# Kernel tuning notes

Measured on AMD Instinct MI355X. Metric: run time of the kernel, lower is better.

The kernel has to match this reference:

```python
import jax, jax.numpy as jnp
import numpy as np

B, N, DIM, H, DH = 2, 1024, 1024, 8, 64
DI = H * DH  # 512
K = 4        # depthwise conv kernel
EPS = 1.1920929e-07  # float32 eps (torch RMSNorm default)


def setup_inputs() -> dict:
    key = jax.random.key(0)
    ks = jax.random.split(key, 12)
    s = lambda k, shape, sc=0.02: jax.random.normal(k, shape, jnp.float32) * sc
    return dict(
        x=jax.random.normal(ks[0], (B, N, DIM), jnp.float32),
        w_rms=jnp.ones((DIM,), jnp.float32),
        wq=s(ks[1], (DIM, DI)), wk=s(ks[2], (DIM, DI)), wv=s(ks[3], (DIM, DI)),
        wo=s(ks[4], (DI, DIM)),
        conv_q=s(ks[5], (DIM, K), 0.3), conv_k=s(ks[6], (DIM, K), 0.3), conv_v=s(ks[7], (DIM, K), 0.3),
        gamma_q=jnp.ones((H, 1, DH), jnp.float32), gamma_k=jnp.ones((H, 1, DH), jnp.float32),
        lr_w=s(ks[8], (DIM, H)), lr_b=jnp.full((H,), -4.0, jnp.float32),
        decay_w=s(ks[9], (DIM, H)), decay_b=jnp.full((H,), 4.0, jnp.float32),
        mom_w=s(ks[10], (DIM, H)), mom_b=jnp.full((H,), 2.0, jnp.float32),
    )


def rmsnorm(x, w):
    return x * jax.lax.rsqrt(jnp.mean(x * x, -1, keepdims=True) + EPS) * w


def mh_rmsnorm(x, gamma):  # x: (b, h, n, d)
    rms = jnp.sqrt(jnp.sum(x * x, -1, keepdims=True)) * (DH ** -0.5)
    return x / jnp.maximum(rms, 1e-8) * gamma


def dwconv(x, w):  # x: (b, n, dim), w: (dim, K) depthwise, padding K//2 -> length n+1
    y = jax.lax.conv_general_dilated(
        x.transpose(0, 2, 1), w[:, None, :], (1,), [(K // 2, K // 2)],
        feature_group_count=DIM, dimension_numbers=('NCW', 'OIW', 'NCW'))
    return y.transpose(0, 2, 1)


def gated_scan(a, x):  # h_t = a_t h_{t-1} + x_t, h_{-1}=0; a:(bh,t), x:(bh,t,d,d)
    def combine(c1, c2):
        a1, x1 = c1
        a2, x2 = c2
        return a1 * a2, a2 * x1 + x2
    _, h = jax.lax.associative_scan(combine, (a[..., None, None], x), axis=1)
    return h


def reference(x, w_rms, wq, wk, wv, wo, conv_q, conv_k, conv_v,
              gamma_q, gamma_k, lr_w, lr_b, decay_w, decay_b, mom_w, mom_b):
    b, n, _ = x.shape
    xa = rmsnorm(x, w_rms)
    qi, ki, vi = dwconv(xa, conv_q), dwconv(xa, conv_k), dwconv(xa, conv_v)
    split = lambda t: t.reshape(b, -1, H, DH).transpose(0, 2, 1, 3)[:, :, :n]  # (b,h,n,d)
    q = mh_rmsnorm(split(qi @ wq), gamma_q)
    k = mh_rmsnorm(split(ki @ wk), gamma_k)
    v = split(vi @ wv)
    fq = q.reshape(b * H, n, DH)
    fk = k.reshape(b * H, n, DH)
    fv = v.reshape(b * H, n, DH)
    sig = jax.nn.sigmoid
    lr = sig(xa @ lr_w + lr_b).transpose(0, 2, 1).reshape(b * H, n)
    decay = sig(xa @ decay_w + decay_b).transpose(0, 2, 1).reshape(b * H, n)
    mom = sig(xa @ mom_w + mom_b).transpose(0, 2, 1).reshape(b * H, n)
    # S_ref = S0 = 0 (fresh state) => pred = 0, delta_vec = -v
    g = jnp.einsum('bti,btj->btij', -fv, fk)          # (bh, n, d, d)
    Z = gated_scan(mom, g)                             # momentum scan
    S = gated_scan(decay, -lr[..., None, None] * Z)    # memory scan
    S_prev = jnp.concatenate([jnp.zeros_like(S[:, :1]), S[:, :-1]], axis=1)
    y = jnp.einsum('btdp,btp->btd', S_prev, fq)        # retrieval y_t = S_{t-1} psi_t
    y = y.reshape(b, H, n, DH).transpose(0, 2, 1, 3).reshape(b, n, DI)
    return y @ wo
```

## Files before the change

kernel.cpp:

```cpp
#include <hip/hip_runtime.h>
#include <math.h>

#define DEV __device__ __forceinline__

constexpr int Bb   = 2;
constexpr int Seq  = 1024;
constexpr int Dim  = 1024;
constexpr int Hh   = 8;
constexpr int Dh   = 64;
constexpr int Di   = 512;
constexpr int BN   = Bb * Seq;
constexpr int NSEQ = Bb * Hh;
constexpr int CHUNK = 32;
constexpr int CLEN  = Seq / CHUNK;
constexpr float EPSV = 1.1920929e-07f;
constexpr int NT2  = 8;
constexpr int KSPL = 8;

typedef _Float16 half8 __attribute__((ext_vector_type(8)));
typedef float    f32x4 __attribute__((ext_vector_type(4)));

DEV float bf2f(unsigned short u) {
  union { unsigned int i; float f; } x; x.i = ((unsigned int)u) << 16; return x.f;
}
DEV unsigned short f2bf(float f) {
  union { float f; unsigned int i; } x; x.f = f;
  unsigned int r = x.i + 0x7fffu + ((x.i >> 16) & 1u);
  return (unsigned short)(r >> 16);
}
DEV float ldin(const void* p, int f32, size_t i) {
  if (f32) return ((const float*)p)[i];
  return bf2f(((const unsigned short*)p)[i]);
}
DEV void ld4(const void* p, int f32, size_t i, float* dst) {
  if (f32) {
    float4 u = *(const float4*)((const float*)p + i);
    dst[0] = u.x; dst[1] = u.y; dst[2] = u.z; dst[3] = u.w;
  } else {
    ushort4 u = *(const ushort4*)((const unsigned short*)p + i);
    dst[0] = bf2f(u.x); dst[1] = bf2f(u.y); dst[2] = bf2f(u.z); dst[3] = bf2f(u.w);
  }
}
DEV int sniff_vote(const void* p, int n, int tid) {
  int j = 2 * tid, valid = 0, bad = 0;
  if (j < n) {
    valid = 1;
    float v = bf2f(((const unsigned short*)p)[j]);
    float a = fabsf(v);
    if (!(a >= 1e-12f && a <= 1e4f)) bad = 1;
  }
#pragma unroll
  for (int m = 1; m < 64; m <<= 1) { valid += __shfl_xor(valid, m); bad += __shfl_xor(bad, m); }
  return (2 * bad > valid) ? 1 : 0;
}

DEV void gld16(const _Float16* g, _Float16* l) {
  __builtin_amdgcn_global_load_lds(
      (const __attribute__((address_space(1))) void*)g,
      (__attribute__((address_space(3))) void*)l, 16, 0, 0);
}

struct InPtrs { const void* p[17]; int n[17]; };

__global__ __launch_bounds__(256) void k_front(
    InPtrs ip,
    int* __restrict__ flags,
    _Float16* __restrict__ wqT, _Float16* __restrict__ wkT,
    _Float16* __restrict__ wvT, _Float16* __restrict__ woT,
    _Float16* __restrict__ WgT,
    float* __restrict__ gqf, float* __restrict__ gkf, float* __restrict__ gbf,
    _Float16* __restrict__ xaf,
    _Float16* __restrict__ qc, _Float16* __restrict__ kc,
    _Float16* __restrict__ vc)
{
  int blk = blockIdx.x;
  int tid = threadIdx.x;
  __shared__ int sfl[8];
  __shared__ __align__(16) char smem_u[11 * Dim * 2];

  if (blk < 1024) {
    int z = blk >> 8, bx = blk & 15, by = (blk >> 4) & 15;
    int idx = (z == 0) ? 2 : ((z == 1) ? 3 : ((z == 2) ? 4 : 5));
    const void* src = ip.p[idx];
    _Float16* dst   = (z == 0) ? wqT : ((z == 1) ? wkT : ((z == 2) ? wvT : woT));
    int Kd = (z < 3) ? Dim : Di;
    int Nn = (z < 3) ? Di : Dim;
    int n0 = bx * 64, k0 = by * 64;
    if (n0 >= Nn || k0 >= Kd) return;

    if (tid < 64) { int f = sniff_vote(src, ip.n[idx], tid); if (tid == 0) sfl[0] = f; }
    __syncthreads();
    int f = sfl[0];

    float (*tile)[65] = (float(*)[65])smem_u;
    int r = tid >> 4, c4 = (tid & 15) * 4;
#pragma unroll
    for (int rr = 0; rr < 4; ++rr) {
      int k = rr * 16 + r;
      ld4(src, f, (size_t)(k0 + k) * Nn + n0 + c4, &tile[k][c4]);
    }
    __syncthreads();
#pragma unroll
    for (int rr = 0; rr < 4; ++rr) {
      int n = rr * 16 + r;
      _Float16 o4[4];
#pragma unroll
      for (int j = 0; j < 4; ++j) o4[j] = (_Float16)tile[c4 + j][n];
      *(ushort4*)&dst[(size_t)(n0 + n) * Kd + k0 + c4] = *(ushort4*)o4;
    }
  } else if (blk < 1088) {
    int row = blk - 1024;
    if (row < 24) {
      int g = row >> 3, h = row & 7;
      int idx = (g == 0) ? 11 : ((g == 1) ? 13 : 15);
      const void* W = ip.p[idx];
      if (tid < 64) { int f = sniff_vote(W, ip.n[idx], tid); if (tid == 0) sfl[0] = f; }
      __syncthreads();
      int f = sfl[0];
#pragma unroll
      for (int it = 0; it < 4; ++it) {
        int d = it * 256 + tid;
        WgT[(size_t)row * Dim + d] = (_Float16)ldin(W, f, (size_t)d * Hh + h);
      }
    } else {
#pragma unroll
      for (int it = 0; it < 4; ++it)
        WgT[(size_t)row * Dim + it * 256 + tid] = (_Float16)0.f;
    }
  } else if (blk == 1088) {
    __shared__ int allf[17];
    for (int ii = 0; ii < 17; ++ii) {
      if (tid < 64) {
        int f = sniff_vote(ip.p[ii], ip.n[ii], tid);
        if (tid == 0) { flags[ii] = f; allf[ii] = f; }
      }
    }
    __syncthreads();
    int f9 = allf[9], f10 = allf[10];
    for (int i = tid; i < Di; i += 256) {
      gqf[i] = ldin(ip.p[9], f9, i);
      gkf[i] = ldin(ip.p[10], f10, i);
    }
    if (tid < 24) {
      int g = tid >> 3, h = tid & 7;
      int idx = (g == 0) ? 12 : ((g == 1) ? 14 : 16);
      gbf[tid] = ldin(ip.p[idx], allf[idx], h);
    }
  } else {
    constexpr int NR = NT2 + 3;
    _Float16 (*xas)[Dim] = (_Float16(*)[Dim])smem_u;

    int rb = blk - 1089;
    int tb = rb & 127, b = rb >> 7;
    int t0 = tb * NT2;
    int lane = tid & 63, wv = tid >> 6;

    if (tid < 64) {
      int f0 = sniff_vote(ip.p[0], ip.n[0], tid);
      int f1 = sniff_vote(ip.p[1], ip.n[1], tid);
      int f6 = sniff_vote(ip.p[6], ip.n[6], tid);
      int f7 = sniff_vote(ip.p[7], ip.n[7], tid);
      int f8 = sniff_vote(ip.p[8], ip.n[8], tid);
      if (tid == 0) { sfl[0] = f0; sfl[1] = f1; sfl[2] = f6; sfl[3] = f7; sfl[4] = f8; }
    }
    __syncthreads();
    int fx = sfl[0], fw = sfl[1], f6 = sfl[2], f7 = sfl[3], f8 = sfl[4];
    int e0 = lane * 16;

    float wr[16];
#pragma unroll
    for (int q = 0; q < 4; ++q) ld4(ip.p[1], fw, e0 + q * 4, &wr[q * 4]);

    for (int rr = wv; rr < NR; rr += 4) {
      int r = t0 - 2 + rr;
      float xv[16];
      bool inr = (r >= 0 && r < Seq);
      if (inr) {
        size_t rbx = (size_t)(b * Seq + r) * Dim + e0;
#pragma unroll
        for (int q = 0; q < 4; ++q) ld4(ip.p[0], fx, rbx + q * 4, &xv[q * 4]);
      } else {
#pragma unroll
        for (int j = 0; j < 16; ++j) xv[j] = 0.f;
      }
      float ss = 0.f;
#pragma unroll
      for (int j = 0; j < 16; ++j) ss = fmaf(xv[j], xv[j], ss);
#pragma unroll
      for (int m = 1; m < 64; m <<= 1) ss += __shfl_xor(ss, m);
      float scale = rsqrtf(ss * (1.0f / Dim) + EPSV);

      _Float16 o[16];
#pragma unroll
      for (int j = 0; j < 16; ++j) o[j] = (_Float16)(xv[j] * scale * wr[j]);
      *(uint4*)&xas[rr][e0]     = *(uint4*)&o[0];
      *(uint4*)&xas[rr][e0 + 8] = *(uint4*)&o[8];
      if (inr && r >= t0 && r < t0 + NT2) {
        size_t ob = (size_t)(b * Seq + r) * Dim + e0;
        *(uint4*)&xaf[ob]     = *(uint4*)&o[0];
        *(uint4*)&xaf[ob + 8] = *(uint4*)&o[8];
      }
    }
    __syncthreads();

    int c0 = tid * 4;
    float lwq[16], lwk[16], lwv[16];
#pragma unroll
    for (int q = 0; q < 4; ++q) {
      ld4(ip.p[6], f6, (size_t)c0 * 4 + q * 4, &lwq[q * 4]);
      ld4(ip.p[7], f7, (size_t)c0 * 4 + q * 4, &lwk[q * 4]);
      ld4(ip.p[8], f8, (size_t)c0 * 4 + q * 4, &lwv[q * 4]);
    }

#pragma unroll
    for (int tt = 0; tt < NT2; ++tt) {
      float rv[4][4];
#pragma unroll
      for (int k = 0; k < 4; ++k) {
        _Float16 hx[4];
        *(ushort4*)hx = *(const ushort4*)&xas[tt + k][c0];
#pragma unroll
        for (int j = 0; j < 4; ++j) rv[k][j] = (float)hx[j];
      }
      _Float16 tq[4], tk[4], tv[4];
#pragma unroll
      for (int j = 0; j < 4; ++j) {
        float aq = rv[0][j] * lwq[j * 4 + 0] + rv[1][j] * lwq[j * 4 + 1]
                 + rv[2][j] * lwq[j * 4 + 2] + rv[3][j] * lwq[j * 4 + 3];
        float ak = rv[0][j] * lwk[j * 4 + 0] + rv[1][j] * lwk[j * 4 + 1]
                 + rv[2][j] * lwk[j * 4 + 2] + rv[3][j] * lwk[j * 4 + 3];
        float av = rv[0][j] * lwv[j * 4 + 0] + rv[1][j] * lwv[j * 4 + 1]
                 + rv[2][j] * lwv[j * 4 + 2] + rv[3][j] * lwv[j * 4 + 3];
        tq[j] = (_Float16)aq; tk[j] = (_Float16)ak; tv[j] = (_Float16)av;
      }
      size_t o = ((size_t)(b * Seq + t0 + tt)) * Dim + c0;
      *(ushort4*)&qc[o] = *(ushort4*)tq;
      *(ushort4*)&kc[o] = *(ushort4*)tk;
      *(ushort4*)&vc[o] = *(ushort4*)tv;
    }
  }
}

__global__ __launch_bounds__(256) void k_mid(
    const _Float16* __restrict__ qc, const _Float16* __restrict__ kc,
    const _Float16* __restrict__ vc,
    const _Float16* __restrict__ wqT, const _Float16* __restrict__ wkT,
    const _Float16* __restrict__ wvT,
    const _Float16* __restrict__ xaf, const _Float16* __restrict__ WgT,
    _Float16* __restrict__ qpre, _Float16* __restrict__ kpre,
    _Float16* __restrict__ vpre,
    float* __restrict__ gpart)
{
  __shared__ __align__(16) _Float16 ldsbuf[256 * 64];

  int blk = blockIdx.x;
  int tid = threadIdx.x, lane = tid & 63, wv = tid >> 6;
  int mrow = lane & 15, quad = lane >> 4;

  if (blk < 192) {
    int z = blk >> 6, rem = blk & 63;
    int by = rem >> 2, bx = rem & 3;
    const _Float16* A  = (z == 0) ? qc : ((z == 1) ? kc : vc);
    const _Float16* Bt = (z == 0) ? wqT : ((z == 1) ? wkT : wvT);
    _Float16* C        = (z == 0) ? qpre : ((z == 1) ? kpre : vpre);
    int m0 = by * 128, n0 = bx * 128;
    int wr = wv >> 1, wc = wv & 1;

    _Float16* Asl = ldsbuf;
    _Float16* Bsl = ldsbuf + 128 * 64;

    int sr8 = lane >> 3;
    int sc8 = (lane & 7) * 8;

    f32x4 acc[4][4];
#pragma unroll
    for (int mi = 0; mi < 4; ++mi)
#pragma unroll
      for (int ni = 0; ni < 4; ++ni) acc[mi][ni] = (f32x4){0.f, 0.f, 0.f, 0.f};

    for (int kt = 0; kt < Dim; kt += 64) {
      __syncthreads();
#pragma unroll
      for (int u = 0; u < 4; ++u) {
        int r0 = wv * 32 + u * 8;
        gld16(&A [(size_t)(m0 + r0 + sr8) * Dim + kt + sc8], &Asl[r0 * 64]);
        gld16(&Bt[(size_t)(n0 + r0 + sr8) * Dim + kt + sc8], &Bsl[r0 * 64]);
      }
      __syncthreads();

#pragma unroll
      for (int kh = 0; kh < 2; ++kh) {
        half8 afr[4], bfr[4];
#pragma unroll
        for (int i = 0; i < 4; ++i)
          afr[i] = *(const half8*)&Asl[(wr * 64 + i * 16 + mrow) * 64 + kh * 32 + quad * 8];
#pragma unroll
        for (int i = 0; i < 4; ++i)
          bfr[i] = *(const half8*)&Bsl[(wc * 64 + i * 16 + mrow) * 64 + kh * 32 + quad * 8];
#pragma unroll
        for (int mi = 0; mi < 4; ++mi)
#pragma unroll
          for (int ni = 0; ni < 4; ++ni)
            acc[mi][ni] = __builtin_amdgcn_mfma_f32_16x16x32_f16(afr[mi], bfr[ni], acc[mi][ni], 0, 0, 0);
      }
    }

#pragma unroll
    for (int mi = 0; mi < 4; ++mi) {
#pragma unroll
      for (int ni = 0; ni < 4; ++ni) {
        int col = n0 + wc * 64 + ni * 16 + mrow;
#pragma unroll
        for (int r2 = 0; r2 < 4; ++r2) {
          int row = m0 + wr * 64 + mi * 16 + quad * 4 + r2;
          C[(size_t)row * Di + col] = (_Float16)acc[mi][ni][r2];
        }
      }
    }
  } else {
    _Float16 (*As)[40] = (_Float16(*)[40])ldsbuf;
    _Float16 (*Bs)[40] = (_Float16(*)[40])(ldsbuf + 128 * 40);

    int g = blk - 192;
    int m0 = (g & 31) * 64, ks = g >> 5;
    int srow = tid >> 2, scol = (tid & 3) * 8;
    int kbase = ks * (Dim / KSPL);

    f32x4 acc[4];
#pragma unroll
    for (int mi = 0; mi < 4; ++mi) acc[mi] = (f32x4){0.f, 0.f, 0.f, 0.f};

    for (int kt = kbase; kt < kbase + Dim / KSPL; kt += 32) {
      __syncthreads();
      *(uint4*)&As[srow][scol] = *(const uint4*)&xaf[(size_t)(m0 + srow) * Dim + kt + scol];
      *(uint4*)&Bs[srow][scol] = *(const uint4*)&WgT[(size_t)srow * Dim + kt + scol];
      __syncthreads();
      half8 bfr = *(const half8*)&Bs[wv * 16 + mrow][quad * 8];
#pragma unroll
      for (int mi = 0; mi < 4; ++mi) {
        half8 afr = *(const half8*)&As[mi * 16 + mrow][quad * 8];
        acc[mi] = __builtin_amdgcn_mfma_f32_16x16x32_f16(afr, bfr, acc[mi], 0, 0, 0);
      }
    }

    int col = wv * 16 + mrow;
    if (col < 24) {
#pragma unroll
      for (int mi = 0; mi < 4; ++mi) {
#pragma unroll
        for (int r2 = 0; r2 < 4; ++r2) {
          int row = m0 + mi * 16 + quad * 4 + r2;
          gpart[((size_t)ks * BN + row) * 32 + col] = acc[mi][r2];
        }
      }
    }
  }
}

__global__ __launch_bounds__(256) void k_gemm_fin(
    const _Float16* __restrict__ A, const _Float16* __restrict__ Bt,
    void* __restrict__ C, const int* __restrict__ flags, int Nn, int Kd)
{
  __shared__ __align__(16) _Float16 lds[(64 + 64) * 32];
  _Float16* Asl = lds;
  _Float16* Bsl = lds + 64 * 32;

  int tid = threadIdx.x, lane = tid & 63, wv = tid >> 6;
  int n0 = blockIdx.x * 64, m0 = blockIdx.y * 64;
  int mrow = lane & 15, quad = lane >> 4;
  int wr = wv >> 1, wc = wv & 1;
  int sr = lane >> 2, sc = (lane & 3) * 8;

  f32x4 acc[2][2];
#pragma unroll
  for (int mi = 0; mi < 2; ++mi)
#pragma unroll
    for (int ni = 0; ni < 2; ++ni) acc[mi][ni] = (f32x4){0.f, 0.f, 0.f, 0.f};

  for (int kt = 0; kt < Kd; kt += 32) {
    __syncthreads();
    gld16(&A [(size_t)(m0 + wv * 16 + sr) * Kd + kt + sc], &Asl[(wv * 16) * 32]);
    gld16(&Bt[(size_t)(n0 + wv * 16 + sr) * Kd + kt + sc], &Bsl[(wv * 16) * 32]);
    __syncthreads();

    half8 afr[2], bfr[2];
#pragma unroll
    for (int i2 = 0; i2 < 2; ++i2) {
      afr[i2] = *(const half8*)&Asl[(wr * 32 + i2 * 16 + mrow) * 32 + quad * 8];
      bfr[i2] = *(const half8*)&Bsl[(wc * 32 + i2 * 16 + mrow) * 32 + quad * 8];
    }
#pragma unroll
    for (int mi = 0; mi < 2; ++mi)
#pragma unroll
      for (int ni = 0; ni < 2; ++ni)
        acc[mi][ni] = __builtin_amdgcn_mfma_f32_16x16x32_f16(afr[mi], bfr[ni], acc[mi][ni], 0, 0, 0);
  }

  int any_bf16 = 0;
#pragma unroll
  for (int i2 = 0; i2 < 17; ++i2) any_bf16 |= (flags[i2] == 0);

#pragma unroll
  for (int mi = 0; mi < 2; ++mi) {
#pragma unroll
    for (int ni = 0; ni < 2; ++ni) {
      int col = n0 + wc * 32 + ni * 16 + mrow;
#pragma unroll
      for (int r2 = 0; r2 < 4; ++r2) {
        int row = m0 + wr * 32 + mi * 16 + quad * 4 + r2;
        float v = acc[mi][ni][r2];
        size_t idx = (size_t)row * Nn + col;
        if (any_bf16) ((unsigned short*)C)[idx] = f2bf(v);
        else          ((float*)C)[idx] = v;
      }
    }
  }
}

DEV void load_gates(const float* __restrict__ gpart, const float* __restrict__ gbf,
                    int b, int h, int c, int tid,
                    float* gl, float* gd, float* gm)
{
  if (tid < 96) {
    int which = tid >> 5, t2 = tid & 31;
    int col = which * 8 + h;
    int row = b * Seq + c * CLEN + t2;
    float acc = gbf[col];
#pragma unroll
    for (int ks = 0; ks < KSPL; ++ks)
      acc += gpart[((size_t)ks * BN + row) * 32 + col];
    float sg = 1.f / (1.f + expf(-acc));
    if (which == 0) gl[t2] = sg; else if (which == 1) gd[t2] = sg; else gm[t2] = sg;
  }
}

__global__ __launch_bounds__(256) void k_phaseA(
    _Float16* __restrict__ kpre, const _Float16* __restrict__ vpre,
    const float* __restrict__ gkf,
    const float* __restrict__ gpart, const float* __restrict__ gbf,
    _Float16* __restrict__ ZS_Z, _Float16* __restrict__ ZS_S,
    float* __restrict__ Mc, float* __restrict__ Dc, float* __restrict__ Wc)
{
  int c = blockIdx.x, s = blockIdx.y;
  int b = s >> 3, h = s & 7;
  int tid = threadIdx.x, lane = tid & 63, wv = tid >> 6;
  int i = tid >> 2, j0 = (tid & 3) * 16;
  __shared__ float kn[CLEN][64], vv[CLEN][64];
  __shared__ float gl[CLEN], gd[CLEN], gm[CLEN];

  {
    int t = tid >> 3, col = (tid & 7) * 8;
    size_t g = ((size_t)(b * Seq + c * CLEN + t)) * Di + h * 64 + col;
    half8 kv = *(const half8*)&kpre[g];
    half8 vvv = *(const half8*)&vpre[g];
#pragma unroll
    for (int j = 0; j < 8; ++j) { kn[t][col + j] = (float)kv[j]; vv[t][col + j] = (float)vvv[j]; }
    load_gates(gpart, gbf, b, h, c, tid, gl, gd, gm);
  }
  __syncthreads();
  {
    float gk = gkf[h * 64 + lane];
#pragma unroll
    for (int tt = 0; tt < 8; ++tt) {
      int t = wv * 8 + tt;
      float kvv = kn[t][lane];
      float ss = kvv * kvv;
#pragma unroll
      for (int m = 1; m < 64; m <<= 1) ss += __shfl_xor(ss, m);
      float knv = kvv * (1.f / fmaxf(sqrtf(ss) * 0.125f, 1e-8f)) * gk;
      kn[t][lane] = knv;
      kpre[((size_t)(b * Seq + c * CLEN + t)) * Di + h * 64 + lane] = (_Float16)knv;
    }
  }
  __syncthreads();

  float Zl[16], Sl[16];
#pragma unroll
  for (int jj = 0; jj < 16; ++jj) { Zl[jj] = 0.f; Sl[jj] = 0.f; }
  float Mcum = 1.f, Dcum = 1.f, wacc = 0.f;

  for (int t = 0; t < CLEN; ++t) {
    float l = gl[t], dd = gd[t], mm = gm[t];
    float vi = vv[t][i];
    Mcum *= mm;
#pragma unroll
    for (int jj = 0; jj < 16; ++jj) {
      Zl[jj] = fmaf(mm, Zl[jj], -vi * kn[t][j0 + jj]);
      Sl[jj] = fmaf(dd, Sl[jj], -l * Zl[jj]);
    }
    wacc = fmaf(dd, wacc, -l * Mcum);
    Dcum *= dd;
  }
  size_t base = ((size_t)(s * CHUNK + c)) * 4096 + (size_t)i * 64 + j0;
  half8 zo0, zo1, so0, so1;
#pragma unroll
  for (int jj = 0; jj < 8; ++jj) {
    zo0[jj] = (_Float16)Zl[jj];     zo1[jj] = (_Float16)Zl[jj + 8];
    so0[jj] = (_Float16)Sl[jj];     so1[jj] = (_Float16)Sl[jj + 8];
  }
  *(half8*)&ZS_Z[base] = zo0; *(half8*)&ZS_Z[base + 8] = zo1;
  *(half8*)&ZS_S[base] = so0; *(half8*)&ZS_S[base + 8] = so1;
  if (tid == 0) {
    Mc[s * CHUNK + c] = Mcum; Dc[s * CHUNK + c] = Dcum; Wc[s * CHUNK + c] = wacc;
  }
}

__global__ __launch_bounds__(256) void k_phaseB(
    _Float16* __restrict__ ZS_Z, _Float16* __restrict__ ZS_S,
    const float* __restrict__ Mc, const float* __restrict__ Dc,
    const float* __restrict__ Wc)
{
  int s = blockIdx.x;
  int e0 = blockIdx.y * 128;
  int tid = threadIdx.x;
  __shared__ _Float16 zbuf[CHUNK][128], sbuf[CHUNK][128];
  __shared__ float gms[3][CHUNK];

  {
#pragma unroll
    for (int r = 0; r < 2; ++r) {
      int idx = r * 256 + tid;
      int c = idx >> 4, es = (idx & 15) * 8;
      size_t g = ((size_t)(s * CHUNK + c)) * 4096 + e0 + es;
      *(half8*)&zbuf[c][es] = *(const half8*)&ZS_Z[g];
      *(half8*)&sbuf[c][es] = *(const half8*)&ZS_S[g];
    }
    if (tid < 96) {
      int w = tid >> 5, c = tid & 31;
      const float* src = (w == 0) ? Mc : ((w == 1) ? Dc : Wc);
      gms[w][c] = src[s * CHUNK + c];
    }
  }
  __syncthreads();

  if (tid < 128) {
    float Z = 0.f, S = 0.f;
#pragma unroll
    for (int c = 0; c < CHUNK; ++c) {
      float zl = (float)zbuf[c][tid], sl = (float)sbuf[c][tid];
      zbuf[c][tid] = (_Float16)Z; sbuf[c][tid] = (_Float16)S;
      float mc = gms[0][c], dc = gms[1][c], wc = gms[2][c];
      S = fmaf(dc, S, fmaf(wc, Z, sl));
      Z = fmaf(mc, Z, zl);
    }
  }
  __syncthreads();

#pragma unroll
  for (int r = 0; r < 2; ++r) {
    int idx = r * 256 + tid;
    int c = idx >> 4, es = (idx & 15) * 8;
    size_t g = ((size_t)(s * CHUNK + c)) * 4096 + e0 + es;
    *(half8*)&ZS_Z[g] = *(const half8*)&zbuf[c][es];
    *(half8*)&ZS_S[g] = *(const half8*)&sbuf[c][es];
  }
}

__global__ __launch_bounds__(256) void k_phaseC(
    const _Float16* __restrict__ qpre, const _Float16* __restrict__ kpre,
    const _Float16* __restrict__ vpre,
    const float* __restrict__ gqf,
    const float* __restrict__ gpart, const float* __restrict__ gbf,
    const _Float16* __restrict__ ZS_Z, const _Float16* __restrict__ ZS_S,
    _Float16* __restrict__ yb)
{
  int c = blockIdx.x, s = blockIdx.y;
  int b = s >> 3, h = s & 7;
  int tid = threadIdx.x, lane = tid & 63, wv = tid >> 6;
  int i = tid >> 2, j0 = (tid & 3) * 16;
  __shared__ float kn[CLEN][64], vv[CLEN][64], qn[CLEN][64];
  __shared__ float gl[CLEN], gd[CLEN], gm[CLEN];

  float Zi_[16], Si_[16], Zl[16], Sl[16];
  size_t base = ((size_t)(s * CHUNK + c)) * 4096 + (size_t)i * 64 + j0;
  {
    half8 z0 = *(const half8*)&ZS_Z[base], z1 = *(const half8*)&ZS_Z[base + 8];
    half8 s0 = *(const half8*)&ZS_S[base], s1 = *(const half8*)&ZS_S[base + 8];
#pragma unroll
    for (int jj = 0; jj < 8; ++jj) {
      Zi_[jj] = (float)z0[jj]; Zi_[jj + 8] = (float)z1[jj];
      Si_[jj] = (float)s0[jj]; Si_[jj + 8] = (float)s1[jj];
      Zl[jj] = 0.f; Zl[jj + 8] = 0.f; Sl[jj] = 0.f; Sl[jj + 8] = 0.f;
    }
  }
  {
    int t = tid >> 3, col = (tid & 7) * 8;
    size_t g = ((size_t)(b * Seq + c * CLEN + t)) * Di + h * 64 + col;
    half8 kv = *(const half8*)&kpre[g];
    half8 vvv = *(const half8*)&vpre[g];
    half8 qv = *(const half8*)&qpre[g];
#pragma unroll
    for (int j = 0; j < 8; ++j) {
      kn[t][col + j] = (float)kv[j]; vv[t][col + j] = (float)vvv[j];
      qn[t][col + j] = (float)qv[j];
    }
    load_gates(gpart, gbf, b, h, c, tid, gl, gd, gm);
  }
  __syncthreads();
  {
    float gq = gqf[h * 64 + lane];
#pragma unroll
    for (int tt = 0; tt < 8; ++tt) {
      int t = wv * 8 + tt;
      float qvv = qn[t][lane];
      float ssq = qvv * qvv;
#pragma unroll
      for (int m = 1; m < 64; m <<= 1) ssq += __shfl_xor(ssq, m);
      qn[t][lane] = qvv * (1.f / fmaxf(sqrtf(ssq) * 0.125f, 1e-8f)) * gq;
    }
  }
  __syncthreads();

  float Mcum = 1.f, Dcum = 1.f, wacc = 0.f;
  float Dprev = 1.f, wprev = 0.f;

  for (int t = 0; t < CLEN; ++t) {
    float l = gl[t], dd = gd[t], mm = gm[t];

    float yp = 0.f;
#pragma unroll
    for (int jj = 0; jj < 16; ++jj) {
      float tmp = fmaf(Dprev, Si_[jj], fmaf(wprev, Zi_[jj], Sl[jj]));
      yp = fmaf(tmp, qn[t][j0 + jj], yp);
    }
    yp += __shfl_xor(yp, 1);
    yp += __shfl_xor(yp, 2);
    if ((tid & 3) == 0)
      yb[((size_t)(b * Seq + c * CLEN + t)) * Di + h * 64 + i] = (_Float16)yp;

    float vi = vv[t][i];
    Mcum *= mm;
#pragma unroll
    for (int jj = 0; jj < 16; ++jj) {
      Zl[jj] = fmaf(mm, Zl[jj], -vi * kn[t][j0 + jj]);
      Sl[jj] = fmaf(dd, Sl[jj], -l * Zl[jj]);
    }
    wacc = fmaf(dd, wacc, -l * Mcum);
    Dcum *= dd;
    Dprev = Dcum; wprev = wacc;
  }
}

extern "C" void kernel_launch(void* const* d_in, const int* in_sizes, int n_in,
                              void* d_out, int out_size, void* d_ws, size_t ws_size,
                              hipStream_t stream) {
  InPtrs ip;
  for (int i = 0; i < 17; ++i) { ip.p[i] = d_in[i]; ip.n[i] = in_sizes[i]; }

  char* p = (char*)d_ws;
  auto take = [&](size_t bytes) -> char* {
    char* q = p; p += (bytes + 255) & ~(size_t)255; return q;
  };
  int* flags           = (int*)take(32 * 4);
  _Float16* xaf        = (_Float16*)take((size_t)BN * Dim * 2);
  _Float16* qc         = (_Float16*)take((size_t)BN * Dim * 2);
  _Float16* kc         = (_Float16*)take((size_t)BN * Dim * 2);
  _Float16* vc         = (_Float16*)take((size_t)BN * Dim * 2);
  _Float16* qpre       = (_Float16*)take((size_t)BN * Di * 2);
  _Float16* kpre       = (_Float16*)take((size_t)BN * Di * 2);
  _Float16* vpre       = (_Float16*)take((size_t)BN * Di * 2);
  float* gpart         = (float*)take((size_t)KSPL * BN * 32 * 4);
  float* Mc            = (float*)take((size_t)NSEQ * CHUNK * 4);
  float* Dc            = (float*)take((size_t)NSEQ * CHUNK * 4);
  float* Wc            = (float*)take((size_t)NSEQ * CHUNK * 4);
  _Float16* wqT        = (_Float16*)take((size_t)Di * Dim * 2);
  _Float16* wkT        = (_Float16*)take((size_t)Di * Dim * 2);
  _Float16* wvT        = (_Float16*)take((size_t)Di * Dim * 2);
  _Float16* woT        = (_Float16*)take((size_t)Dim * Di * 2);
  _Float16* WgT        = (_Float16*)take((size_t)64 * Dim * 2);
  float* gqf           = (float*)take(Di * 4);
  float* gkf           = (float*)take(Di * 4);
  float* gbf           = (float*)take(32 * 4);
  _Float16* ZS_Z       = qc;
  _Float16* ZS_S       = kc;
  _Float16* yb         = vc;

  k_front<<<1345, 256, 0, stream>>>(ip, flags, wqT, wkT, wvT, woT, WgT,
                                    gqf, gkf, gbf, xaf, qc, kc, vc);

  k_mid<<<448, 256, 0, stream>>>(qc, kc, vc, wqT, wkT, wvT, xaf, WgT,
                                 qpre, kpre, vpre, gpart);

  k_phaseA<<<dim3(CHUNK, NSEQ), 256, 0, stream>>>(kpre, vpre, gkf,
                                                  gpart, gbf,
                                                  ZS_Z, ZS_S, Mc, Dc, Wc);
  k_phaseB<<<dim3(NSEQ, 4096 / 128), 256, 0, stream>>>(ZS_Z, ZS_S, Mc, Dc, Wc);
  k_phaseC<<<dim3(CHUNK, NSEQ), 256, 0, stream>>>(qpre, kpre, vpre, gqf,
                                                  gpart, gbf,
                                                  ZS_Z, ZS_S, yb);

  k_gemm_fin<<<dim3(Dim / 64, BN / 64), 256, 0, stream>>>(
      yb, woT, d_out, flags, Dim, Di);
}
```

Before: 178.0 us.

## Fuse chunk-scan phases and output GEMM into one persistent kernel with grid barriers

Merges phaseA, phaseB, phaseC and the final output projection GEMM into one 512-block kernel. The stages are separated by atomic grid-wide barriers instead of separate kernel launches. The fused kernel keeps the normalized k, v and q chunk data in shared memory between phase A and phase C, so they are loaded and normalized once instead of twice. This removes three launch gaps and one reload of the chunk data. In exchange it depends on all 512 blocks being resident at once (launch_bounds of 2 blocks per CU), or the barriers deadlock, and spin-waiting adds barrier latency.

```diff
diff --git a/kernel.cpp b/kernel.cpp
--- a/kernel.cpp
+++ b/kernel.cpp
@@ -16,6 +16,7 @@
 constexpr float EPSV = 1.1920929e-07f;
 constexpr int NT2  = 8;
 constexpr int KSPL = 8;
+constexpr int NBACK = 512;
 
 typedef _Float16 half8 __attribute__((ext_vector_type(8)));
 typedef float    f32x4 __attribute__((ext_vector_type(4)));
@@ -58,6 +59,19 @@
   __builtin_amdgcn_global_load_lds(
       (const __attribute__((address_space(1))) void*)g,
       (__attribute__((address_space(3))) void*)l, 16, 0, 0);
+}
+
+DEV void gbar(int* bar, int nb) {
+  __syncthreads();
+  if (threadIdx.x == 0) {
+    __threadfence();
+    __hip_atomic_fetch_add(bar, 1, __ATOMIC_ACQ_REL, __HIP_MEMORY_SCOPE_AGENT);
+    while (__hip_atomic_load(bar, __ATOMIC_ACQUIRE, __HIP_MEMORY_SCOPE_AGENT) < nb) {
+      __builtin_amdgcn_s_sleep(16);
+    }
+  }
+  __syncthreads();
+  __threadfence();
 }
 
 struct InPtrs { const void* p[17]; int n[17]; };
@@ -249,13 +263,15 @@
     const _Float16* __restrict__ xaf, const _Float16* __restrict__ WgT,
     _Float16* __restrict__ qpre, _Float16* __restrict__ kpre,
     _Float16* __restrict__ vpre,
-    float* __restrict__ gpart)
+    float* __restrict__ gpart, int* __restrict__ bars)
 {
   __shared__ __align__(16) _Float16 ldsbuf[256 * 64];
 
   int blk = blockIdx.x;
   int tid = threadIdx.x, lane = tid & 63, wv = tid >> 6;
   int mrow = lane & 15, quad = lane >> 4;
+
+  if (blk == 0 && tid < 16) bars[tid] = 0;
 
   if (blk < 192) {
     int z = blk >> 6, rem = blk & 63;
@@ -352,66 +368,6 @@
           int row = m0 + mi * 16 + quad * 4 + r2;
           gpart[((size_t)ks * BN + row) * 32 + col] = acc[mi][r2];
         }
-      }
-    }
-  }
-}
-
-__global__ __launch_bounds__(256) void k_gemm_fin(
-    const _Float16* __restrict__ A, const _Float16* __restrict__ Bt,
-    void* __restrict__ C, const int* __restrict__ flags, int Nn, int Kd)
-{
-  __shared__ __align__(16) _Float16 lds[(64 + 64) * 32];
-  _Float16* Asl = lds;
-  _Float16* Bsl = lds + 64 * 32;
-
-  int tid = threadIdx.x, lane = tid & 63, wv = tid >> 6;
-  int n0 = blockIdx.x * 64, m0 = blockIdx.y * 64;
-  int mrow = lane & 15, quad = lane >> 4;
-  int wr = wv >> 1, wc = wv & 1;
-  int sr = lane >> 2, sc = (lane & 3) * 8;
-
-  f32x4 acc[2][2];
-#pragma unroll
-  for (int mi = 0; mi < 2; ++mi)
-#pragma unroll
-    for (int ni = 0; ni < 2; ++ni) acc[mi][ni] = (f32x4){0.f, 0.f, 0.f, 0.f};
-
-  for (int kt = 0; kt < Kd; kt += 32) {
-    __syncthreads();
-    gld16(&A [(size_t)(m0 + wv * 16 + sr) * Kd + kt + sc], &Asl[(wv * 16) * 32]);
-    gld16(&Bt[(size_t)(n0 + wv * 16 + sr) * Kd + kt + sc], &Bsl[(wv * 16) * 32]);
-    __syncthreads();
-
-    half8 afr[2], bfr[2];
-#pragma unroll
-    for (int i2 = 0; i2 < 2; ++i2) {
-      afr[i2] = *(const half8*)&Asl[(wr * 32 + i2 * 16 + mrow) * 32 + quad * 8];
-      bfr[i2] = *(const half8*)&Bsl[(wc * 32 + i2 * 16 + mrow) * 32 + quad * 8];
-    }
-#pragma unroll
-    for (int mi = 0; mi < 2; ++mi)
-#pragma unroll
-      for (int ni = 0; ni < 2; ++ni)
-        acc[mi][ni] = __builtin_amdgcn_mfma_f32_16x16x32_f16(afr[mi], bfr[ni], acc[mi][ni], 0, 0, 0);
-  }
-
-  int any_bf16 = 0;
-#pragma unroll
-  for (int i2 = 0; i2 < 17; ++i2) any_bf16 |= (flags[i2] == 0);
-
-#pragma unroll
-  for (int mi = 0; mi < 2; ++mi) {
-#pragma unroll
-    for (int ni = 0; ni < 2; ++ni) {
-      int col = n0 + wc * 32 + ni * 16 + mrow;
-#pragma unroll
-      for (int r2 = 0; r2 < 4; ++r2) {
-        int row = m0 + wr * 32 + mi * 16 + quad * 4 + r2;
-        float v = acc[mi][ni][r2];
-        size_t idx = (size_t)row * Nn + col;
-        if (any_bf16) ((unsigned short*)C)[idx] = f2bf(v);
-        else          ((float*)C)[idx] = v;
       }
     }
   }
@@ -434,155 +390,31 @@
   }
 }
 
-__global__ __launch_bounds__(256) void k_phaseA(
-    _Float16* __restrict__ kpre, const _Float16* __restrict__ vpre,
-    const float* __restrict__ gkf,
+__global__ __launch_bounds__(256, 2) void k_back(
+    const _Float16* __restrict__ qpre, const _Float16* __restrict__ kpre,
+    const _Float16* __restrict__ vpre,
+    const float* __restrict__ gqf, const float* __restrict__ gkf,
     const float* __restrict__ gpart, const float* __restrict__ gbf,
     _Float16* __restrict__ ZS_Z, _Float16* __restrict__ ZS_S,
-    float* __restrict__ Mc, float* __restrict__ Dc, float* __restrict__ Wc)
+    float* __restrict__ Mc, float* __restrict__ Dc, float* __restrict__ Wc,
+    _Float16* __restrict__ yb, const _Float16* __restrict__ woT,
+    void* __restrict__ Cout, const int* __restrict__ flags,
+    int* __restrict__ bars)
 {
-  int c = blockIdx.x, s = blockIdx.y;
-  int b = s >> 3, h = s & 7;
-  int tid = threadIdx.x, lane = tid & 63, wv = tid >> 6;
-  int i = tid >> 2, j0 = (tid & 3) * 16;
-  __shared__ float kn[CLEN][64], vv[CLEN][64];
-  __shared__ float gl[CLEN], gd[CLEN], gm[CLEN];
-
-  {
-    int t = tid >> 3, col = (tid & 7) * 8;
-    size_t g = ((size_t)(b * Seq + c * CLEN + t)) * Di + h * 64 + col;
-    half8 kv = *(const half8*)&kpre[g];
-    half8 vvv = *(const half8*)&vpre[g];
-#pragma unroll
-    for (int j = 0; j < 8; ++j) { kn[t][col + j] = (float)kv[j]; vv[t][col + j] = (float)vvv[j]; }
-    load_gates(gpart, gbf, b, h, c, tid, gl, gd, gm);
-  }
-  __syncthreads();
-  {
-    float gk = gkf[h * 64 + lane];
-#pragma unroll
-    for (int tt = 0; tt < 8; ++tt) {
-      int t = wv * 8 + tt;
-      float kvv = kn[t][lane];
-      float ss = kvv * kvv;
-#pragma unroll
-      for (int m = 1; m < 64; m <<= 1) ss += __shfl_xor(ss, m);
-      float knv = kvv * (1.f / fmaxf(sqrtf(ss) * 0.125f, 1e-8f)) * gk;
-      kn[t][lane] = knv;
-      kpre[((size_t)(b * Seq + c * CLEN + t)) * Di + h * 64 + lane] = (_Float16)knv;
-    }
-  }
-  __syncthreads();
-
-  float Zl[16], Sl[16];
-#pragma unroll
-  for (int jj = 0; jj < 16; ++jj) { Zl[jj] = 0.f; Sl[jj] = 0.f; }
-  float Mcum = 1.f, Dcum = 1.f, wacc = 0.f;
-
-  for (int t = 0; t < CLEN; ++t) {
-    float l = gl[t], dd = gd[t], mm = gm[t];
-    float vi = vv[t][i];
-    Mcum *= mm;
-#pragma unroll
-    for (int jj = 0; jj < 16; ++jj) {
-      Zl[jj] = fmaf(mm, Zl[jj], -vi * kn[t][j0 + jj]);
-      Sl[jj] = fmaf(dd, Sl[jj], -l * Zl[jj]);
-    }
-    wacc = fmaf(dd, wacc, -l * Mcum);
-    Dcum *= dd;
-  }
-  size_t base = ((size_t)(s * CHUNK + c)) * 4096 + (size_t)i * 64 + j0;
-  half8 zo0, zo1, so0, so1;
-#pragma unroll
-  for (int jj = 0; jj < 8; ++jj) {
-    zo0[jj] = (_Float16)Zl[jj];     zo1[jj] = (_Float16)Zl[jj + 8];
-    so0[jj] = (_Float16)Sl[jj];     so1[jj] = (_Float16)Sl[jj + 8];
-  }
-  *(half8*)&ZS_Z[base] = zo0; *(half8*)&ZS_Z[base + 8] = zo1;
-  *(half8*)&ZS_S[base] = so0; *(half8*)&ZS_S[base + 8] = so1;
-  if (tid == 0) {
-    Mc[s * CHUNK + c] = Mcum; Dc[s * CHUNK + c] = Dcum; Wc[s * CHUNK + c] = wacc;
-  }
-}
-
-__global__ __launch_bounds__(256) void k_phaseB(
-    _Float16* __restrict__ ZS_Z, _Float16* __restrict__ ZS_S,
-    const float* __restrict__ Mc, const float* __restrict__ Dc,
-    const float* __restrict__ Wc)
-{
-  int s = blockIdx.x;
-  int e0 = blockIdx.y * 128;
-  int tid = threadIdx.x;
-  __shared__ _Float16 zbuf[CHUNK][128], sbuf[CHUNK][128];
-  __shared__ float gms[3][CHUNK];
-
-  {
-#pragma unroll
-    for (int r = 0; r < 2; ++r) {
-      int idx = r * 256 + tid;
-      int c = idx >> 4, es = (idx & 15) * 8;
-      size_t g = ((size_t)(s * CHUNK + c)) * 4096 + e0 + es;
-      *(half8*)&zbuf[c][es] = *(const half8*)&ZS_Z[g];
-      *(half8*)&sbuf[c][es] = *(const half8*)&ZS_S[g];
-    }
-    if (tid < 96) {
-      int w = tid >> 5, c = tid & 31;
-      const float* src = (w == 0) ? Mc : ((w == 1) ? Dc : Wc);
-      gms[w][c] = src[s * CHUNK + c];
-    }
-  }
-  __syncthreads();
-
-  if (tid < 128) {
-    float Z = 0.f, S = 0.f;
-#pragma unroll
-    for (int c = 0; c < CHUNK; ++c) {
-      float zl = (float)zbuf[c][tid], sl = (float)sbuf[c][tid];
-      zbuf[c][tid] = (_Float16)Z; sbuf[c][tid] = (_Float16)S;
-      float mc = gms[0][c], dc = gms[1][c], wc = gms[2][c];
-      S = fmaf(dc, S, fmaf(wc, Z, sl));
-      Z = fmaf(mc, Z, zl);
-    }
-  }
-  __syncthreads();
-
-#pragma unroll
-  for (int r = 0; r < 2; ++r) {
-    int idx = r * 256 + tid;
-    int c = idx >> 4, es = (idx & 15) * 8;
-    size_t g = ((size_t)(s * CHUNK + c)) * 4096 + e0 + es;
-    *(half8*)&ZS_Z[g] = *(const half8*)&zbuf[c][es];
-    *(half8*)&ZS_S[g] = *(const half8*)&sbuf[c][es];
-  }
-}
-
-__global__ __launch_bounds__(256) void k_phaseC(
-    const _Float16* __restrict__ qpre, const _Float16* __restrict__ kpre,
-    const _Float16* __restrict__ vpre,
-    const float* __restrict__ gqf,
-    const float* __restrict__ gpart, const float* __restrict__ gbf,
-    const _Float16* __restrict__ ZS_Z, const _Float16* __restrict__ ZS_S,
-    _Float16* __restrict__ yb)
-{
-  int c = blockIdx.x, s = blockIdx.y;
-  int b = s >> 3, h = s & 7;
-  int tid = threadIdx.x, lane = tid & 63, wv = tid >> 6;
-  int i = tid >> 2, j0 = (tid & 3) * 16;
   __shared__ float kn[CLEN][64], vv[CLEN][64], qn[CLEN][64];
   __shared__ float gl[CLEN], gd[CLEN], gm[CLEN];
-
-  float Zi_[16], Si_[16], Zl[16], Sl[16];
-  size_t base = ((size_t)(s * CHUNK + c)) * 4096 + (size_t)i * 64 + j0;
-  {
-    half8 z0 = *(const half8*)&ZS_Z[base], z1 = *(const half8*)&ZS_Z[base + 8];
-    half8 s0 = *(const half8*)&ZS_S[base], s1 = *(const half8*)&ZS_S[base + 8];
-#pragma unroll
-    for (int jj = 0; jj < 8; ++jj) {
-      Zi_[jj] = (float)z0[jj]; Zi_[jj + 8] = (float)z1[jj];
-      Si_[jj] = (float)s0[jj]; Si_[jj + 8] = (float)s1[jj];
-      Zl[jj] = 0.f; Zl[jj + 8] = 0.f; Sl[jj] = 0.f; Sl[jj + 8] = 0.f;
-    }
-  }
+  __shared__ __align__(16) _Float16 zbuf[CHUNK][128];
+  __shared__ __align__(16) _Float16 sbuf[CHUNK][128];
+  __shared__ float gms[3][CHUNK];
+
+  int bid = blockIdx.x;
+  int tid = threadIdx.x, lane = tid & 63, wv = tid >> 6;
+
+  int c = bid & 31, s = bid >> 5;
+  int b = s >> 3, h = s & 7;
+  int i = tid >> 2, j0 = (tid & 3) * 16;
+  size_t zsbase = ((size_t)(s * CHUNK + c)) * 4096 + (size_t)i * 64 + j0;
+
   {
     int t = tid >> 3, col = (tid & 7) * 8;
     size_t g = ((size_t)(b * Seq + c * CLEN + t)) * Di + h * 64 + col;
@@ -598,46 +430,196 @@
   }
   __syncthreads();
   {
+    float gk = gkf[h * 64 + lane];
     float gq = gqf[h * 64 + lane];
 #pragma unroll
     for (int tt = 0; tt < 8; ++tt) {
       int t = wv * 8 + tt;
+      float kvv = kn[t][lane];
+      float ssk = kvv * kvv;
       float qvv = qn[t][lane];
       float ssq = qvv * qvv;
 #pragma unroll
-      for (int m = 1; m < 64; m <<= 1) ssq += __shfl_xor(ssq, m);
+      for (int m = 1; m < 64; m <<= 1) { ssk += __shfl_xor(ssk, m); ssq += __shfl_xor(ssq, m); }
+      kn[t][lane] = kvv * (1.f / fmaxf(sqrtf(ssk) * 0.125f, 1e-8f)) * gk;
       qn[t][lane] = qvv * (1.f / fmaxf(sqrtf(ssq) * 0.125f, 1e-8f)) * gq;
     }
   }
   __syncthreads();
 
-  float Mcum = 1.f, Dcum = 1.f, wacc = 0.f;
-  float Dprev = 1.f, wprev = 0.f;
-
-  for (int t = 0; t < CLEN; ++t) {
-    float l = gl[t], dd = gd[t], mm = gm[t];
-
-    float yp = 0.f;
-#pragma unroll
-    for (int jj = 0; jj < 16; ++jj) {
-      float tmp = fmaf(Dprev, Si_[jj], fmaf(wprev, Zi_[jj], Sl[jj]));
-      yp = fmaf(tmp, qn[t][j0 + jj], yp);
-    }
-    yp += __shfl_xor(yp, 1);
-    yp += __shfl_xor(yp, 2);
-    if ((tid & 3) == 0)
-      yb[((size_t)(b * Seq + c * CLEN + t)) * Di + h * 64 + i] = (_Float16)yp;
-
-    float vi = vv[t][i];
-    Mcum *= mm;
-#pragma unroll
-    for (int jj = 0; jj < 16; ++jj) {
-      Zl[jj] = fmaf(mm, Zl[jj], -vi * kn[t][j0 + jj]);
-      Sl[jj] = fmaf(dd, Sl[jj], -l * Zl[jj]);
-    }
-    wacc = fmaf(dd, wacc, -l * Mcum);
-    Dcum *= dd;
-    Dprev = Dcum; wprev = wacc;
+  {
+    float Zl[16], Sl[16];
+#pragma unroll
+    for (int jj = 0; jj < 16; ++jj) { Zl[jj] = 0.f; Sl[jj] = 0.f; }
+    float Mcum = 1.f, Dcum = 1.f, wacc = 0.f;
+
+    for (int t = 0; t < CLEN; ++t) {
+      float l = gl[t], dd = gd[t], mm = gm[t];
+      float vi = vv[t][i];
+      Mcum *= mm;
+#pragma unroll
+      for (int jj = 0; jj < 16; ++jj) {
+        Zl[jj] = fmaf(mm, Zl[jj], -vi * kn[t][j0 + jj]);
+        Sl[jj] = fmaf(dd, Sl[jj], -l * Zl[jj]);
+      }
+      wacc = fmaf(dd, wacc, -l * Mcum);
+      Dcum *= dd;
+    }
+    half8 zo0, zo1, so0, so1;
+#pragma unroll
+    for (int jj = 0; jj < 8; ++jj) {
+      zo0[jj] = (_Float16)Zl[jj];     zo1[jj] = (_Float16)Zl[jj + 8];
+      so0[jj] = (_Float16)Sl[jj];     so1[jj] = (_Float16)Sl[jj + 8];
+    }
+    *(half8*)&ZS_Z[zsbase] = zo0; *(half8*)&ZS_Z[zsbase + 8] = zo1;
+    *(half8*)&ZS_S[zsbase] = so0; *(half8*)&ZS_S[zsbase + 8] = so1;
+    if (tid == 0) {
+      Mc[s * CHUNK + c] = Mcum; Dc[s * CHUNK + c] = Dcum; Wc[s * CHUNK + c] = wacc;
+    }
+  }
+
+  gbar(&bars[0], NBACK);
+
+  {
+    int sB = bid & 15;
+    int e0 = (bid >> 4) * 128;
+#pragma unroll
+    for (int r = 0; r < 2; ++r) {
+      int idx = r * 256 + tid;
+      int cc = idx >> 4, es = (idx & 15) * 8;
+      size_t g = ((size_t)(sB * CHUNK + cc)) * 4096 + e0 + es;
+      *(half8*)&zbuf[cc][es] = *(const half8*)&ZS_Z[g];
+      *(half8*)&sbuf[cc][es] = *(const half8*)&ZS_S[g];
+    }
+    if (tid < 96) {
+      int w = tid >> 5, cc = tid & 31;
+      const float* src = (w == 0) ? Mc : ((w == 1) ? Dc : Wc);
+      gms[w][cc] = src[sB * CHUNK + cc];
+    }
+    __syncthreads();
+
+    if (tid < 128) {
+      float Z = 0.f, S = 0.f;
+#pragma unroll
+      for (int cc = 0; cc < CHUNK; ++cc) {
+        float zl = (float)zbuf[cc][tid], sl = (float)sbuf[cc][tid];
+        zbuf[cc][tid] = (_Float16)Z; sbuf[cc][tid] = (_Float16)S;
+        float mc = gms[0][cc], dc = gms[1][cc], wc = gms[2][cc];
+        S = fmaf(dc, S, fmaf(wc, Z, sl));
+        Z = fmaf(mc, Z, zl);
+      }
+    }
+    __syncthreads();
+
+#pragma unroll
+    for (int r = 0; r < 2; ++r) {
+      int idx = r * 256 + tid;
+      int cc = idx >> 4, es = (idx & 15) * 8;
+      size_t g = ((size_t)(sB * CHUNK + cc)) * 4096 + e0 + es;
+      *(half8*)&ZS_Z[g] = *(const half8*)&zbuf[cc][es];
+      *(half8*)&ZS_S[g] = *(const half8*)&sbuf[cc][es];
+    }
+  }
+
+  gbar(&bars[1], NBACK);
+
+  {
+    float Zi_[16], Si_[16], Zl[16], Sl[16];
+    {
+      half8 z0 = *(const half8*)&ZS_Z[zsbase], z1 = *(const half8*)&ZS_Z[zsbase + 8];
+      half8 s0 = *(const half8*)&ZS_S[zsbase], s1 = *(const half8*)&ZS_S[zsbase + 8];
+#pragma unroll
+      for (int jj = 0; jj < 8; ++jj) {
+        Zi_[jj] = (float)z0[jj]; Zi_[jj + 8] = (float)z1[jj];
+        Si_[jj] = (float)s0[jj]; Si_[jj + 8] = (float)s1[jj];
+        Zl[jj] = 0.f; Zl[jj + 8] = 0.f; Sl[jj] = 0.f; Sl[jj + 8] = 0.f;
+      }
+    }
+
+    float Mcum = 1.f, Dcum = 1.f, wacc = 0.f;
+    float Dprev = 1.f, wprev = 0.f;
+
+    for (int t = 0; t < CLEN; ++t) {
+      float l = gl[t], dd = gd[t], mm = gm[t];
+
+      float yp = 0.f;
+#pragma unroll
+      for (int jj = 0; jj < 16; ++jj) {
+        float tmp = fmaf(Dprev, Si_[jj], fmaf(wprev, Zi_[jj], Sl[jj]));
+        yp = fmaf(tmp, qn[t][j0 + jj], yp);
+      }
+      yp += __shfl_xor(yp, 1);
+      yp += __shfl_xor(yp, 2);
+      if ((tid & 3) == 0)
+        yb[((size_t)(b * Seq + c * CLEN + t)) * Di + h * 64 + i] = (_Float16)yp;
+
+      float vi = vv[t][i];
+      Mcum *= mm;
+#pragma unroll
+      for (int jj = 0; jj < 16; ++jj) {
+        Zl[jj] = fmaf(mm, Zl[jj], -vi * kn[t][j0 + jj]);
+        Sl[jj] = fmaf(dd, Sl[jj], -l * Zl[jj]);
+      }
+      wacc = fmaf(dd, wacc, -l * Mcum);
+      Dcum *= dd;
+      Dprev = Dcum; wprev = wacc;
+    }
+  }
+
+  gbar(&bars[2], NBACK);
+
+  {
+    _Float16* Asl = (_Float16*)zbuf;
+    _Float16* Bsl = (_Float16*)sbuf;
+    int m0 = (bid >> 4) * 64, n0 = (bid & 15) * 64;
+    int mrow = lane & 15, quad = lane >> 4;
+    int wr = wv >> 1, wc = wv & 1;
+    int sr = lane >> 2, sc = (lane & 3) * 8;
+
+    f32x4 acc[2][2];
+#pragma unroll
+    for (int mi = 0; mi < 2; ++mi)
+#pragma unroll
+      for (int ni = 0; ni < 2; ++ni) acc[mi][ni] = (f32x4){0.f, 0.f, 0.f, 0.f};
+
+    for (int kt = 0; kt < Di; kt += 32) {
+      __syncthreads();
+      gld16(&yb [(size_t)(m0 + wv * 16 + sr) * Di + kt + sc], &Asl[(wv * 16) * 32]);
+      gld16(&woT[(size_t)(n0 + wv * 16 + sr) * Di + kt + sc], &Bsl[(wv * 16) * 32]);
+      __syncthreads();
+
+      half8 afr[2], bfr[2];
+#pragma unroll
+      for (int i2 = 0; i2 < 2; ++i2) {
+        afr[i2] = *(const half8*)&Asl[(wr * 32 + i2 * 16 + mrow) * 32 + quad * 8];
+        bfr[i2] = *(const half8*)&Bsl[(wc * 32 + i2 * 16 + mrow) * 32 + quad * 8];
+      }
+#pragma unroll
+      for (int mi = 0; mi < 2; ++mi)
+#pragma unroll
+        for (int ni = 0; ni < 2; ++ni)
+          acc[mi][ni] = __builtin_amdgcn_mfma_f32_16x16x32_f16(afr[mi], bfr[ni], acc[mi][ni], 0, 0, 0);
+    }
+
+    int any_bf16 = 0;
+#pragma unroll
+    for (int i2 = 0; i2 < 17; ++i2) any_bf16 |= (flags[i2] == 0);
+
+#pragma unroll
+    for (int mi = 0; mi < 2; ++mi) {
+#pragma unroll
+      for (int ni = 0; ni < 2; ++ni) {
+        int col = n0 + wc * 32 + ni * 16 + mrow;
+#pragma unroll
+        for (int r2 = 0; r2 < 4; ++r2) {
+          int row = m0 + wr * 32 + mi * 16 + quad * 4 + r2;
+          float v = acc[mi][ni][r2];
+          size_t idx = (size_t)row * Dim + col;
+          if (any_bf16) ((unsigned short*)Cout)[idx] = f2bf(v);
+          else          ((float*)Cout)[idx] = v;
+        }
+      }
+    }
   }
 }
 
@@ -652,6 +634,7 @@
     char* q = p; p += (bytes + 255) & ~(size_t)255; return q;
   };
   int* flags           = (int*)take(32 * 4);
+  int* bars            = (int*)take(16 * 4);
   _Float16* xaf        = (_Float16*)take((size_t)BN * Dim * 2);
   _Float16* qc         = (_Float16*)take((size_t)BN * Dim * 2);
   _Float16* kc         = (_Float16*)take((size_t)BN * Dim * 2);
@@ -679,16 +662,9 @@
                                     gqf, gkf, gbf, xaf, qc, kc, vc);
 
   k_mid<<<448, 256, 0, stream>>>(qc, kc, vc, wqT, wkT, wvT, xaf, WgT,
-                                 qpre, kpre, vpre, gpart);
-
-  k_phaseA<<<dim3(CHUNK, NSEQ), 256, 0, stream>>>(kpre, vpre, gkf,
-                                                  gpart, gbf,
-                                                  ZS_Z, ZS_S, Mc, Dc, Wc);
-  k_phaseB<<<dim3(NSEQ, 4096 / 128), 256, 0, stream>>>(ZS_Z, ZS_S, Mc, Dc, Wc);
-  k_phaseC<<<dim3(CHUNK, NSEQ), 256, 0, stream>>>(qpre, kpre, vpre, gqf,
-                                                  gpart, gbf,
-                                                  ZS_Z, ZS_S, yb);
-
-  k_gemm_fin<<<dim3(Dim / 64, BN / 64), 256, 0, stream>>>(
-      yb, woT, d_out, flags, Dim, Di);
-}
+                                 qpre, kpre, vpre, gpart, bars);
+
+  k_back<<<NBACK, 256, 0, stream>>>(qpre, kpre, vpre, gqf, gkf,
+                                    gpart, gbf, ZS_Z, ZS_S, Mc, Dc, Wc,
+                                    yb, woT, d_out, flags, bars);
+}
```

Measured after the change: 411.2 us. 131% more time.
